# Optimization experiments

Hardware: AMD Instinct MI355X
Metric: run time of the kernel (lower is better)

## Reference

```python
import jax, jax.numpy as jnp
import numpy as np

DIM = 2048
HV = 32          # num value heads
HK = 16          # num key heads
DK = 128         # head_k_dim
DV = 128         # head_v_dim
KW = 4           # conv kernel width
KEY_DIM = HK * DK            # 2048
VAL_DIM = HV * DV            # 4096
CONV_DIM = 2 * KEY_DIM + VAL_DIM  # 8192
EPS = 1e-6
B, T = 2, 2048


def setup_inputs() -> dict:
    key = jax.random.key(0)
    ks = jax.random.split(key, 10)
    s = 0.02
    x = jax.random.normal(ks[0], (B, T, DIM), jnp.float32)
    W_qkv = jax.random.normal(ks[1], (DIM, CONV_DIM), jnp.float32) * s
    W_z = jax.random.normal(ks[2], (DIM, VAL_DIM), jnp.float32) * s
    W_a = jax.random.normal(ks[3], (DIM, HV), jnp.float32) * s
    W_b = jax.random.normal(ks[4], (DIM, HV), jnp.float32) * s
    W_out = jax.random.normal(ks[5], (VAL_DIM, DIM), jnp.float32) * s
    conv_w = jax.random.normal(ks[6], (CONV_DIM, KW), jnp.float32) * 0.2
    A_log = jnp.log(jax.random.uniform(ks[7], (HV,), jnp.float32, 1e-3, 16.0))
    dt_bias = jnp.ones((HV,), jnp.float32)
    norm_weight = jnp.ones((DV,), jnp.float32)
    return {"x": x, "W_qkv": W_qkv, "W_z": W_z, "W_a": W_a, "W_b": W_b,
            "W_out": W_out, "conv_w": conv_w, "dt_bias": dt_bias,
            "A_log": A_log, "norm_weight": norm_weight}


def _l2norm(t):
    return t * jax.lax.rsqrt(jnp.sum(t * t, axis=-1, keepdims=True) + EPS)


def _forward(x, W_qkv, W_z, W_a, W_b, W_out, conv_w, dt_bias, A_log, norm_weight):
    Bb, Tt, _ = x.shape
    mixed = x @ W_qkv                       # [B,T,CONV_DIM]
    z = x @ W_z                             # [B,T,VAL_DIM]
    a = x @ W_a                             # [B,T,HV]
    b = x @ W_b                             # [B,T,HV]

    # depthwise causal conv1d (left pad KW-1) + silu
    xp = jnp.pad(mixed, ((0, 0), (KW - 1, 0), (0, 0)))
    conv = sum(xp[:, i:i + Tt, :] * conv_w[:, i] for i in range(KW))
    mixed = jax.nn.silu(conv)

    q, k, v = jnp.split(mixed, [KEY_DIM, 2 * KEY_DIM], axis=-1)
    q = q.reshape(Bb, Tt, HK, DK)
    k = k.reshape(Bb, Tt, HK, DK)
    v = v.reshape(Bb, Tt, HV, DV)
    rep = HV // HK
    q = jnp.repeat(q, rep, axis=2)          # [B,T,HV,DK]
    k = jnp.repeat(k, rep, axis=2)

    # decay / beta
    beta = jax.nn.sigmoid(b)                                    # [B,T,HV]
    g = -jnp.exp(A_log) * jax.nn.softplus(a + dt_bias)          # [B,T,HV], < 0

    # qk l2norm in kernel + scale
    q = _l2norm(q) * (DK ** -0.5)
    k = _l2norm(k)

    # gated delta rule recurrence, time-major scan
    qT = q.transpose(1, 0, 2, 3)
    kT = k.transpose(1, 0, 2, 3)
    vT = v.transpose(1, 0, 2, 3)
    gT = g.transpose(1, 0, 2)
    bT = beta.transpose(1, 0, 2)
    S0 = jnp.zeros((Bb, HV, DK, DV), jnp.float32)

    def step(S, inp):
        qt, kt, vt, gt, bt = inp
        S = S * jnp.exp(gt)[..., None, None]
        pred = jnp.einsum('bhk,bhkv->bhv', kt, S)
        u = (vt - pred) * bt[..., None]
        S = S + jnp.einsum('bhk,bhv->bhkv', kt, u)
        o = jnp.einsum('bhk,bhkv->bhv', qt, S)
        return S, o

    _, oT = jax.lax.scan(step, S0, (qT, kT, vT, gT, bT))
    o = oT.transpose(1, 0, 2, 3)            # [B,T,HV,DV]

    # gated RMSNorm over head_v_dim: weight * rmsnorm(o) * silu(z)
    var = jnp.mean(o * o, axis=-1, keepdims=True)
    on = o * jax.lax.rsqrt(var + EPS) * norm_weight
    zg = z.reshape(Bb, Tt, HV, DV)
    on = on * jax.nn.silu(zg)

    return on.reshape(Bb, Tt, VAL_DIM) @ W_out


def reference(x, W_qkv, W_z, W_a, W_b, W_out, conv_w, dt_bias, A_log, norm_weight):
    return _forward(x, W_qkv, W_z, W_a, W_b, W_out, conv_w, dt_bias, A_log, norm_weight)
```

## Files before the change

### kernel.cpp

```cpp
#include <hip/hip_runtime.h>
#include <hip/hip_bf16.h>
#include <cstdint>
#include <cstddef>

#define DIM_ 2048
#define HV_ 32
#define HK_ 16
#define DK_ 128
#define DV_ 128
#define KW_ 4
#define KEY_DIM_ 2048
#define VAL_DIM_ 4096
#define CONV_DIM_ 8192
#define B_ 2
#define T_ 2048
#define BT_ 4096
#define CH_ 64
#define NC_ (T_ / CH_)

typedef short s8v __attribute__((ext_vector_type(8)));
typedef float f4v __attribute__((ext_vector_type(4)));

__device__ __forceinline__ unsigned short f2b(float f) {
    union { float f; unsigned u; } c; c.f = f;
    unsigned u = c.u;
    return (unsigned short)((u + 0x7fffu + ((u >> 16) & 1u)) >> 16);
}
__device__ __forceinline__ float b2f(unsigned short s) {
    union { unsigned u; float f; } c; c.u = ((unsigned)s) << 16;
    return c.f;
}
__device__ __forceinline__ unsigned int pk2(float a, float b) {
    return (unsigned)f2b(a) | ((unsigned)f2b(b) << 16);
}
__device__ __forceinline__ float silu(float x) { return x / (1.f + expf(-x)); }

__global__ void cast_bf16_k(const float* __restrict__ in, unsigned short* __restrict__ out, int n8) {
    int i = blockIdx.x * blockDim.x + threadIdx.x;
    if (i >= n8) return;
    int base = i * 8;
    f4v a = *(const f4v*)(in + base);
    f4v b = *(const f4v*)(in + base + 4);
    s8v o;
    o[0] = (short)f2b(a[0]); o[1] = (short)f2b(a[1]); o[2] = (short)f2b(a[2]); o[3] = (short)f2b(a[3]);
    o[4] = (short)f2b(b[0]); o[5] = (short)f2b(b[1]); o[6] = (short)f2b(b[2]); o[7] = (short)f2b(b[3]);
    *(s8v*)(out + base) = o;
}

__global__ void transpose_cast_k(const float* __restrict__ in, unsigned short* __restrict__ out,
                                 int R, int C) {
    __shared__ float tile[32][33];
    int c0 = blockIdx.x * 32, r0 = blockIdx.y * 32;
    int tx = threadIdx.x & 31, ty = threadIdx.x >> 5;
#pragma unroll
    for (int j = 0; j < 32; j += 8)
        tile[ty + j][tx] = in[(size_t)(r0 + ty + j) * C + c0 + tx];
    __syncthreads();
#pragma unroll
    for (int j = 0; j < 32; j += 8)
        out[(size_t)(c0 + ty + j) * R + r0 + tx] = f2b(tile[tx][ty + j]);
}

__global__ void pack_ab_k(const float* __restrict__ Wa, const float* __restrict__ Wb,
                          float* __restrict__ WabP) {
    int idx = blockIdx.x * 256 + threadIdx.x;
    int k = idx >> 6;
    int c = idx & 63;
    float v = (c < 32) ? Wa[(size_t)k * 32 + c] : Wb[(size_t)k * 32 + (c - 32)];
    WabP[((size_t)(k >> 2) * 64 + c) * 4 + (k & 3)] = v;
}

template <int OUT_BF16>
__global__ __launch_bounds__(256) void gemm_bt_k(const unsigned short* __restrict__ A,
                                                 const unsigned short* __restrict__ BT,
                                                 void* __restrict__ Cv,
                                                 int M, int N, int K) {
    __shared__ __attribute__((aligned(16))) unsigned short As[128 * 64];
    __shared__ __attribute__((aligned(16))) unsigned short Bs[128 * 64];
    const int tid = threadIdx.x;
    const int wid = tid >> 6, lane = tid & 63;
    const int wm = wid >> 1, wn = wid & 1;
    const int m0 = blockIdx.y * 128, n0 = blockIdx.x * 128;

    f4v acc[4][4];
#pragma unroll
    for (int i = 0; i < 4; i++)
#pragma unroll
        for (int j = 0; j < 4; j++) acc[i][j] = (f4v){0.f, 0.f, 0.f, 0.f};

    const int rowA = tid >> 3;
    const int cb   = (tid & 7) << 4;

    for (int kt = 0; kt < K; kt += 64) {
#pragma unroll
        for (int i = 0; i < 4; i++) {
            int row = i * 32 + rowA;
            int scb = cb ^ ((row & 7) << 4);
            const unsigned short* ga = A  + (size_t)(m0 + row) * K + kt + (scb >> 1);
            const unsigned short* gb = BT + (size_t)(n0 + row) * K + kt + (scb >> 1);
            char* la = (char*)As + i * 4096 + (wid << 10);
            char* lb = (char*)Bs + i * 4096 + (wid << 10);
            __builtin_amdgcn_global_load_lds(
                (const __attribute__((address_space(1))) unsigned int*)ga,
                (__attribute__((address_space(3))) unsigned int*)la, 16, 0, 0);
            __builtin_amdgcn_global_load_lds(
                (const __attribute__((address_space(1))) unsigned int*)gb,
                (__attribute__((address_space(3))) unsigned int*)lb, 16, 0, 0);
        }
        __syncthreads();
#pragma unroll
        for (int kk = 0; kk < 2; kk++) {
            s8v af[4], bfr[4];
#pragma unroll
            for (int mi = 0; mi < 4; mi++) {
                int row = wm * 64 + mi * 16 + (lane & 15);
                int byteoff = (row << 7) + ((kk * 64 + ((lane >> 4) << 4)) ^ ((row & 7) << 4));
                af[mi] = *(const s8v*)((const char*)As + byteoff);
            }
#pragma unroll
            for (int ni = 0; ni < 4; ni++) {
                int row = wn * 64 + ni * 16 + (lane & 15);
                int byteoff = (row << 7) + ((kk * 64 + ((lane >> 4) << 4)) ^ ((row & 7) << 4));
                bfr[ni] = *(const s8v*)((const char*)Bs + byteoff);
            }
#pragma unroll
            for (int mi = 0; mi < 4; mi++)
#pragma unroll
                for (int ni = 0; ni < 4; ni++)
                    acc[mi][ni] = __builtin_amdgcn_mfma_f32_16x16x32_bf16(
                        af[mi], bfr[ni], acc[mi][ni], 0, 0, 0);
        }
        __syncthreads();
    }
#pragma unroll
    for (int mi = 0; mi < 4; mi++) {
#pragma unroll
        for (int ni = 0; ni < 4; ni++) {
            int row = m0 + wm * 64 + mi * 16 + ((lane >> 4) << 2);
            int col = n0 + wn * 64 + ni * 16 + (lane & 15);
#pragma unroll
            for (int r = 0; r < 4; r++) {
                float v = acc[mi][ni][r];
                if (OUT_BF16)
                    ((unsigned short*)Cv)[(size_t)(row + r) * N + col] = f2b(v);
                else
                    ((float*)Cv)[(size_t)(row + r) * N + col] = v;
            }
        }
    }
}

__global__ __launch_bounds__(256) void ab_gbeta_k(const float* __restrict__ x,
                                                  const float* __restrict__ WabP,
                                                  const float* __restrict__ dt_bias,
                                                  const float* __restrict__ A_log,
                                                  float* __restrict__ g, float* __restrict__ beta) {
    const int c = threadIdx.x & 63;
    const int rg = __builtin_amdgcn_readfirstlane(threadIdx.x >> 6);
    const int row = blockIdx.x * 4 + rg;
    const float* xp = x + (size_t)row * 2048;
    const float* wp = WabP + c * 4;
    float acc0 = 0.f, acc1 = 0.f;
#pragma unroll 4
    for (int kb = 0; kb < 512; kb += 2) {
        f4v w0 = *(const f4v*)(wp + (size_t)kb * 256);
        f4v w1 = *(const f4v*)(wp + (size_t)(kb + 1) * 256);
        f4v x0 = *(const f4v*)(xp + kb * 4);
        f4v x1 = *(const f4v*)(xp + kb * 4 + 4);
        acc0 += x0[0] * w0[0] + x0[1] * w0[1] + x0[2] * w0[2] + x0[3] * w0[3];
        acc1 += x1[0] * w1[0] + x1[1] * w1[1] + x1[2] * w1[2] + x1[3] * w1[3];
    }
    float tot = acc0 + acc1;
    if (c < 32) {
        float av = tot + dt_bias[c];
        float sp = (av > 20.f) ? av : log1pf(expf(av));
        g[(size_t)row * 32 + c] = -expf(A_log[c]) * sp;
    } else {
        beta[(size_t)row * 32 + (c - 32)] = 1.f / (1.f + expf(-tot));
    }
}

__global__ __launch_bounds__(256) void conv_fused_k(const unsigned short* __restrict__ mixp,
                                                    const float* __restrict__ convw,
                                                    unsigned short* __restrict__ qn,
                                                    unsigned short* __restrict__ kn,
                                                    unsigned short* __restrict__ vv) {
    int btid = blockIdx.x;
    int t = btid & (T_ - 1);
    int c = (blockIdx.y << 9) + (threadIdx.x << 1);
    const unsigned short* base = mixp + (size_t)btid * CONV_DIM_ + c;
    unsigned m3 = *(const unsigned*)(base);
    unsigned m2 = (t >= 1) ? *(const unsigned*)(base - CONV_DIM_) : 0u;
    unsigned m1 = (t >= 2) ? *(const unsigned*)(base - 2 * CONV_DIM_) : 0u;
    unsigned m0 = (t >= 3) ? *(const unsigned*)(base - 3 * CONV_DIM_) : 0u;
    f4v w0 = *(const f4v*)(convw + (size_t)c * 4);
    f4v w1 = *(const f4v*)(convw + (size_t)c * 4 + 4);
    float v0 = b2f((unsigned short)(m3 & 0xffff)) * w0[3] + b2f((unsigned short)(m2 & 0xffff)) * w0[2]
             + b2f((unsigned short)(m1 & 0xffff)) * w0[1] + b2f((unsigned short)(m0 & 0xffff)) * w0[0];
    float v1 = b2f((unsigned short)(m3 >> 16)) * w1[3] + b2f((unsigned short)(m2 >> 16)) * w1[2]
             + b2f((unsigned short)(m1 >> 16)) * w1[1] + b2f((unsigned short)(m0 >> 16)) * w1[0];
    v0 = silu(v0); v1 = silu(v1);
    if (c < 2 * KEY_DIM_) {
        float ss = v0 * v0 + v1 * v1;
#pragma unroll
        for (int m = 1; m < 64; m <<= 1) ss += __shfl_xor(ss, m);
        float scale = rsqrtf(ss + 1e-6f);
        int head = (c >> 7) & 15, d = c & 127;
        if (c < KEY_DIM_) {
            scale *= 0.08838834764831845f;
            *(unsigned*)(qn + ((size_t)btid * HK_ + head) * DK_ + d) = pk2(v0 * scale, v1 * scale);
        } else {
            *(unsigned*)(kn + ((size_t)btid * HK_ + head) * DK_ + d) = pk2(v0 * scale, v1 * scale);
        }
    } else {
        *(unsigned*)(vv + (size_t)btid * VAL_DIM_ + (c - 2 * KEY_DIM_)) = pk2(v0, v1);
    }
}

__global__ __launch_bounds__(256) void chunk_pre_k(
    const unsigned short* __restrict__ qn, const unsigned short* __restrict__ kn,
    unsigned short* __restrict__ vv,
    const float* __restrict__ g, const float* __restrict__ beta,
    unsigned short* __restrict__ Wg, unsigned short* __restrict__ Aog,
    unsigned short* __restrict__ knT, float* __restrict__ expG, float* __restrict__ expGr)
{
    const int c = blockIdx.x, h = blockIdx.y, b = blockIdx.z;
    const int hk = h >> 1;
    const int tid = threadIdx.x, wid = tid >> 6, lane = tid & 63;
    const int r15 = lane & 15, g4 = lane >> 4;

    __shared__ __attribute__((aligned(16))) unsigned short Klds[64 * 128];
    __shared__ __attribute__((aligned(16))) unsigned short Xlds[128 * 64];
    __shared__ float AT[64][68];
    __shared__ float STmp[16][17];
    __shared__ float Gl[64], Bl[64], EG[64];

    const size_t t0 = (size_t)b * T_ + (size_t)c * 64;
    const size_t cbk = ((size_t)(b * 32 + h) * 32 + c);

#pragma unroll
    for (int p = 0; p < 4; p++) {
        int row = p * 16 + (tid >> 4);
        int colB = (tid & 15) << 4;
        int sw = colB ^ ((row & 7) << 4);
        s8v kv = *(const s8v*)(kn + ((t0 + row) * HK_ + hk) * DK_ + (colB >> 1));
        *(s8v*)((char*)Klds + row * 256 + sw) = kv;
        s8v qv = *(const s8v*)(qn + ((t0 + row) * HK_ + hk) * DK_ + (colB >> 1));
        *(s8v*)((char*)Xlds + row * 256 + sw) = qv;
    }
    if (tid < 64) {
        Gl[tid] = g[(t0 + tid) * HV_ + h];
        Bl[tid] = beta[(t0 + tid) * HV_ + h];
    }
    __syncthreads();
    if (tid == 0) {
        float s = 0.f;
        for (int i = 0; i < 64; i++) { s += Gl[i]; Gl[i] = s; }
    }
    __syncthreads();
    if (tid < 64) {
        float Gi = Gl[tid], Gn = Gl[63];
        float e1 = expf(Gi), e2 = expf(Gn - Gi);
        EG[tid] = e1;
        expG[cbk * 64 + tid] = e1;
        expGr[cbk * 64 + tid] = e2;
    }
    __syncthreads();

    f4v kkv[4], qkv[4];
#pragma unroll
    for (int jt = 0; jt < 4; jt++) { kkv[jt] = (f4v){0,0,0,0}; qkv[jt] = (f4v){0,0,0,0}; }
    const int arow = wid * 16 + r15;
#pragma unroll
    for (int ks = 0; ks < 4; ks++) {
        int abyte = arow * 256 + ((ks * 64 + (g4 << 4)) ^ ((arow & 7) << 4));
        s8v ak = *(const s8v*)((const char*)Klds + abyte);
        s8v aq = *(const s8v*)((const char*)Xlds + abyte);
#pragma unroll
        for (int jt = 0; jt < 4; jt++) {
            int jrow = jt * 16 + r15;
            int bbyte = jrow * 256 + ((ks * 64 + (g4 << 4)) ^ ((jrow & 7) << 4));
            s8v bk = *(const s8v*)((const char*)Klds + bbyte);
            kkv[jt] = __builtin_amdgcn_mfma_f32_16x16x32_bf16(ak, bk, kkv[jt], 0, 0, 0);
            qkv[jt] = __builtin_amdgcn_mfma_f32_16x16x32_bf16(aq, bk, qkv[jt], 0, 0, 0);
        }
    }
#pragma unroll
    for (int jt = 0; jt < 4; jt++) {
#pragma unroll
        for (int r = 0; r < 4; r++) {
            int i = wid * 16 + g4 * 4 + r;
            int j = jt * 16 + r15;
            float em = expf(fminf(Gl[i] - Gl[j], 0.f));
            AT[i][j] = (j < i) ? Bl[i] * em * kkv[jt][r] : 0.f;
            float ao = (j <= i) ? em * qkv[jt][r] : 0.f;
            Aog[cbk * 4096 + i * 64 + j] = f2b(ao);
        }
    }
    __syncthreads();

    for (int u = tid; u < 1024; u += 256) {
        int row = u >> 4, v0i = (u & 15) << 3;
        s8v vx = *(const s8v*)(vv + (t0 + row) * VAL_DIM_ + h * 128 + v0i);
        float bt = Bl[row];
#pragma unroll
        for (int e = 0; e < 8; e++) {
            int v = v0i + e;
            *(unsigned short*)((char*)Xlds + v * 128 + ((row * 2) ^ ((v & 7) << 4))) =
                f2b(b2f((unsigned short)vx[e]) * bt);
        }
    }
    if ((h & 1) == 0) {
        int dk = tid & 127, th = (tid >> 7) << 5;
        size_t basek = ((size_t)(b * 16 + hk) * 128 + dk) * (size_t)T_ + (size_t)c * 64 + th;
#pragma unroll
        for (int t8 = 0; t8 < 4; t8++) {
            s8v kv;
#pragma unroll
            for (int e = 0; e < 8; e++) {
                int tt = th + t8 * 8 + e;
                kv[e] = (short)*(const unsigned short*)((const char*)Klds + tt * 256 + ((dk * 2) ^ ((tt & 7) << 4)));
            }
            *(s8v*)(knT + basek + t8 * 8) = kv;
        }
    }
    __syncthreads();

    if (lane < 16) {
        int r0 = wid * 16, col = lane;
#pragma unroll
        for (int i = 0; i < 16; i++) {
            float s = 0.f;
            for (int j = 0; j < i; j++) s += AT[r0 + i][r0 + j] * AT[r0 + j][r0 + col];
            AT[r0 + i][r0 + col] = ((col == i) ? 1.f : 0.f) - s;
        }
    }
    __syncthreads();

    {
        int ii = tid >> 4, jj = tid & 15;
        for (int I = 1; I < 4; I++)
            for (int J = 0; J < I; J++) {
                float s = 0.f;
                for (int K = J; K < I; K++) {
#pragma unroll
                    for (int m = 0; m < 16; m++)
                        s += AT[16 * I + ii][16 * K + m] * AT[16 * K + m][16 * J + jj];
                }
                STmp[ii][jj] = s;
                __syncthreads();
                float y = 0.f;
#pragma unroll
                for (int m = 0; m < 16; m++) y += AT[16 * I + ii][16 * I + m] * STmp[m][jj];
                __syncthreads();
                AT[16 * I + ii][16 * J + jj] = -y;
                __syncthreads();
            }
    }

    f4v tb[8];
#pragma unroll
    for (int vt = 0; vt < 8; vt++) tb[vt] = (f4v){0,0,0,0};
#pragma unroll
    for (int ks = 0; ks < 2; ks++) {
        s8v ta;
#pragma unroll
        for (int e = 0; e < 8; e++) ta[e] = (short)f2b(AT[arow][ks * 32 + g4 * 8 + e]);
#pragma unroll
        for (int vt = 0; vt < 8; vt++) {
            int v = vt * 16 + r15;
            int bbyte = v * 128 + ((ks * 64 + (g4 << 4)) ^ ((v & 7) << 4));
            s8v bv = *(const s8v*)((const char*)Xlds + bbyte);
            tb[vt] = __builtin_amdgcn_mfma_f32_16x16x32_bf16(ta, bv, tb[vt], 0, 0, 0);
        }
    }
#pragma unroll
    for (int vt = 0; vt < 8; vt++)
#pragma unroll
        for (int r = 0; r < 4; r++) {
            int i = wid * 16 + g4 * 4 + r, v = vt * 16 + r15;
            vv[(t0 + i) * VAL_DIM_ + h * 128 + v] = f2b(tb[vt][r]);
        }
    __syncthreads();

    {
        int dk = tid & 127;
        int tb0 = (tid >> 7) << 5;
#pragma unroll
        for (int t8 = 0; t8 < 4; t8++) {
            int tbase = tb0 + t8 * 8;
            s8v kw;
#pragma unroll
            for (int e = 0; e < 8; e++) {
                int t = tbase + e;
                float kv = b2f(*(const unsigned short*)((const char*)Klds + t * 256 + ((dk * 2) ^ ((t & 7) << 4))));
                kw[e] = (short)f2b(kv * Bl[t] * EG[t]);
            }
            *(s8v*)((char*)Xlds + dk * 128 + ((tbase * 2) ^ ((dk & 7) << 4))) = kw;
        }
    }
    __syncthreads();

    f4v wm[8];
#pragma unroll
    for (int dt = 0; dt < 8; dt++) wm[dt] = (f4v){0,0,0,0};
#pragma unroll
    for (int ks = 0; ks < 2; ks++) {
        s8v ta;
#pragma unroll
        for (int e = 0; e < 8; e++) ta[e] = (short)f2b(AT[arow][ks * 32 + g4 * 8 + e]);
#pragma unroll
        for (int dt = 0; dt < 8; dt++) {
            int dkr = dt * 16 + r15;
            int bbyte = dkr * 128 + ((ks * 64 + (g4 << 4)) ^ ((dkr & 7) << 4));
            s8v bw = *(const s8v*)((const char*)Xlds + bbyte);
            wm[dt] = __builtin_amdgcn_mfma_f32_16x16x32_bf16(ta, bw, wm[dt], 0, 0, 0);
        }
    }
#pragma unroll
    for (int dt = 0; dt < 8; dt++)
#pragma unroll
        for (int r = 0; r < 4; r++) {
            int i = wid * 16 + g4 * 4 + r, dk = dt * 16 + r15;
            Wg[cbk * 8192 + i * 128 + dk] = f2b(wm[dt][r]);
        }
}

__global__ __launch_bounds__(256) void chunk_scan_k(
    const unsigned short* __restrict__ qn, const unsigned short* __restrict__ knT,
    const unsigned short* __restrict__ tbv,
    const unsigned short* __restrict__ Wg, const unsigned short* __restrict__ Aog,
    const float* __restrict__ expG, const float* __restrict__ expGr,
    unsigned short* __restrict__ ob)
{
    const int bx = blockIdx.x;
    const int vq = bx & 3, h = (bx >> 2) & 31, b = bx >> 7;
    const int hk = h >> 1;
    const int tid = threadIdx.x, wid = tid >> 6, lane = tid & 63;
    const int r15 = lane & 15, g4 = lane >> 4;

    __shared__ __attribute__((aligned(16))) unsigned short Slds[32 * 128];
    __shared__ __attribute__((aligned(16))) unsigned short Ulds[32 * 64];
    __shared__ __attribute__((aligned(16))) unsigned short Uplds[32 * 64];

    f4v S[2][2];
#pragma unroll
    for (int i = 0; i < 2; i++)
#pragma unroll
        for (int j = 0; j < 2; j++) S[i][j] = (f4v){0,0,0,0};

    struct ScanOps {
        s8v aw[4], aa[2], ak[4], q0[4];
        float tv[8], egr4[4], egi, gam;
    };
    ScanOps opA, opB;

    const unsigned short* kpbase = knT + ((size_t)(b * 16 + hk) * 128) * (size_t)T_;

    auto scan_load = [&](ScanOps& o, int c) {
        const size_t cbk = ((size_t)(b * 32 + h) * 32 + c);
        const size_t t0 = (size_t)b * T_ + (size_t)c * 64;
        const unsigned short* wp = Wg + cbk * 8192 + (size_t)(wid * 16 + r15) * 128;
#pragma unroll
        for (int ks = 0; ks < 4; ks++) o.aw[ks] = *(const s8v*)(wp + ks * 32 + g4 * 8);
        const unsigned short* ap = Aog + cbk * 4096 + (size_t)(wid * 16 + r15) * 64;
#pragma unroll
        for (int ks = 0; ks < 2; ks++) o.aa[ks] = *(const s8v*)(ap + ks * 32 + g4 * 8);
#pragma unroll
        for (int ks = 0; ks < 2; ks++)
#pragma unroll
            for (int dkt = 0; dkt < 2; dkt++)
                o.ak[ks * 2 + dkt] = *(const s8v*)(kpbase +
                    (size_t)((wid * 2 + dkt) * 16 + r15) * T_ + (size_t)c * 64 + ks * 32 + g4 * 8);
        const unsigned short* qp = qn + ((t0 + wid * 16 + r15) * HK_ + hk) * DK_;
#pragma unroll
        for (int ks = 0; ks < 4; ks++) o.q0[ks] = *(const s8v*)(qp + ks * 32 + g4 * 8);
#pragma unroll
        for (int vt = 0; vt < 2; vt++)
#pragma unroll
            for (int r = 0; r < 4; r++) {
                int t = wid * 16 + g4 * 4 + r;
                o.tv[vt * 4 + r] = b2f(tbv[(t0 + t) * VAL_DIM_ + h * 128 + vq * 32 + vt * 16 + r15]);
            }
#pragma unroll
        for (int r = 0; r < 4; r++) o.egr4[r] = expGr[cbk * 64 + wid * 16 + g4 * 4 + r];
        o.egi = expG[cbk * 64 + wid * 16 + r15];
        o.gam = expG[cbk * 64 + 63];
    };

    auto body = [&](ScanOps& o, int c) {
#pragma unroll
        for (int dkt = 0; dkt < 2; dkt++)
#pragma unroll
            for (int vt = 0; vt < 2; vt++) {
                int v = vt * 16 + r15;
                int dkb = ((wid * 2 + dkt) * 16 + g4 * 4) * 2;
                int sw = (v & 7) << 4;
                *(unsigned int*)((char*)Slds + v * 256 + ((dkb) ^ sw))     = pk2(S[dkt][vt][0], S[dkt][vt][1]);
                *(unsigned int*)((char*)Slds + v * 256 + ((dkb + 4) ^ sw)) = pk2(S[dkt][vt][2], S[dkt][vt][3]);
            }
        __syncthreads();

        f4v P[2]; P[0] = (f4v){0,0,0,0}; P[1] = (f4v){0,0,0,0};
        s8v sf[4][2];
#pragma unroll
        for (int ks = 0; ks < 4; ks++)
#pragma unroll
            for (int vt = 0; vt < 2; vt++) {
                int v = vt * 16 + r15;
                sf[ks][vt] = *(const s8v*)((const char*)Slds + v * 256 + ((ks * 64 + g4 * 16) ^ ((v & 7) << 4)));
                P[vt] = __builtin_amdgcn_mfma_f32_16x16x32_bf16(o.aw[ks], sf[ks][vt], P[vt], 0, 0, 0);
            }
#pragma unroll
        for (int vt = 0; vt < 2; vt++) {
            float uu[4], up[4];
#pragma unroll
            for (int r = 0; r < 4; r++) {
                uu[r] = o.tv[vt * 4 + r] - P[vt][r];
                up[r] = uu[r] * o.egr4[r];
            }
            int v = vt * 16 + r15;
            int tb2 = (wid * 16 + g4 * 4) * 2;
            int sw = (v & 7) << 4;
            *(unsigned int*)((char*)Ulds  + v * 128 + ((tb2) ^ sw))     = pk2(uu[0], uu[1]);
            *(unsigned int*)((char*)Ulds  + v * 128 + ((tb2 + 4) ^ sw)) = pk2(uu[2], uu[3]);
            *(unsigned int*)((char*)Uplds + v * 128 + ((tb2) ^ sw))     = pk2(up[0], up[1]);
            *(unsigned int*)((char*)Uplds + v * 128 + ((tb2 + 4) ^ sw)) = pk2(up[2], up[3]);
        }

        f4v O[2]; O[0] = (f4v){0,0,0,0}; O[1] = (f4v){0,0,0,0};
#pragma unroll
        for (int ks = 0; ks < 4; ks++) {
            s8v qg;
#pragma unroll
            for (int e = 0; e < 8; e++) qg[e] = (short)f2b(b2f((unsigned short)o.q0[ks][e]) * o.egi);
#pragma unroll
            for (int vt = 0; vt < 2; vt++)
                O[vt] = __builtin_amdgcn_mfma_f32_16x16x32_bf16(qg, sf[ks][vt], O[vt], 0, 0, 0);
        }
        __syncthreads();

#pragma unroll
        for (int ks = 0; ks < 2; ks++)
#pragma unroll
            for (int vt = 0; vt < 2; vt++) {
                int v = vt * 16 + r15;
                s8v bu = *(const s8v*)((const char*)Ulds + v * 128 + ((ks * 64 + g4 * 16) ^ ((v & 7) << 4)));
                O[vt] = __builtin_amdgcn_mfma_f32_16x16x32_bf16(o.aa[ks], bu, O[vt], 0, 0, 0);
            }
#pragma unroll
        for (int vt = 0; vt < 2; vt++)
#pragma unroll
            for (int r = 0; r < 4; r++) {
                int t = c * 64 + wid * 16 + g4 * 4 + r;
                ob[((size_t)b * T_ + t) * VAL_DIM_ + h * 128 + vq * 32 + vt * 16 + r15] = f2b(O[vt][r]);
            }

#pragma unroll
        for (int dkt = 0; dkt < 2; dkt++)
#pragma unroll
            for (int vt = 0; vt < 2; vt++) {
                S[dkt][vt][0] *= o.gam; S[dkt][vt][1] *= o.gam;
                S[dkt][vt][2] *= o.gam; S[dkt][vt][3] *= o.gam;
            }
#pragma unroll
        for (int ks = 0; ks < 2; ks++) {
            s8v bu[2];
#pragma unroll
            for (int vt = 0; vt < 2; vt++) {
                int v = vt * 16 + r15;
                bu[vt] = *(const s8v*)((const char*)Uplds + v * 128 + ((ks * 64 + g4 * 16) ^ ((v & 7) << 4)));
            }
#pragma unroll
            for (int dkt = 0; dkt < 2; dkt++)
#pragma unroll
                for (int vt = 0; vt < 2; vt++)
                    S[dkt][vt] = __builtin_amdgcn_mfma_f32_16x16x32_bf16(o.ak[ks * 2 + dkt], bu[vt], S[dkt][vt], 0, 0, 0);
        }
    };

    scan_load(opA, 0);
    for (int c = 0; c < NC_; c += 2) {
        scan_load(opB, (c + 1 < NC_) ? c + 1 : c);
        body(opA, c);
        if (c + 2 < NC_) scan_load(opA, c + 2);
        body(opB, c + 1);
    }
}

__global__ __launch_bounds__(256) void norm_gate_k(unsigned short* __restrict__ o,
                                                   const unsigned short* __restrict__ z,
                                                   const float* __restrict__ nw) {
    int lane = threadIdx.x & 63;
    size_t bh = (size_t)blockIdx.x * 4 + (threadIdx.x >> 6);
    unsigned ov = *(unsigned*)(o + bh * 128 + lane * 2);
    float v0 = b2f((unsigned short)(ov & 0xffff)), v1 = b2f((unsigned short)(ov >> 16));
    float ss = v0 * v0 + v1 * v1;
#pragma unroll
    for (int m = 1; m < 64; m <<= 1) ss += __shfl_xor(ss, m);
    float rr = rsqrtf(ss * (1.f / 128.f) + 1e-6f);
    unsigned zv = *(const unsigned*)(z + bh * 128 + lane * 2);
    float z0 = b2f((unsigned short)(zv & 0xffff)), z1 = b2f((unsigned short)(zv >> 16));
    float o0 = v0 * rr * nw[lane * 2]     * silu(z0);
    float o1 = v1 * rr * nw[lane * 2 + 1] * silu(z1);
    *(unsigned*)(o + bh * 128 + lane * 2) = pk2(o0, o1);
}

extern "C" void kernel_launch(void* const* d_in, const int* in_sizes, int n_in,
                              void* d_out, int out_size, void* d_ws, size_t ws_size,
                              hipStream_t stream) {
    const float* x      = (const float*)d_in[0];
    const float* W_qkv  = (const float*)d_in[1];
    const float* W_z    = (const float*)d_in[2];
    const float* W_a    = (const float*)d_in[3];
    const float* W_b    = (const float*)d_in[4];
    const float* W_out  = (const float*)d_in[5];
    const float* conv_w = (const float*)d_in[6];
    const float* dt_bias= (const float*)d_in[7];
    const float* A_log  = (const float*)d_in[8];
    const float* norm_w = (const float*)d_in[9];

    char* w = (char*)d_ws;
    const size_t MBc = (size_t)1 << 20;
    unsigned short* mixp  = (unsigned short*)(w);
    unsigned short* Wmat  = (unsigned short*)(w);
    unsigned short* knT   = (unsigned short*)(w + 32 * MBc);
    unsigned short* Aog   = (unsigned short*)(w + 48 * MBc);
    unsigned short* WqkvT = (unsigned short*)(w + 64 * MBc);
    unsigned short* obuf  = (unsigned short*)(w + 64 * MBc);
    unsigned short* kn    = (unsigned short*)(w + 80 * MBc);
    unsigned short* WzT   = (unsigned short*)(w + 96 * MBc);
    unsigned short* WoutT = (unsigned short*)(w + 96 * MBc);
    unsigned short* xb    = (unsigned short*)(w + 112 * MBc);
    unsigned short* qn    = (unsigned short*)(w + 112 * MBc);
    unsigned short* vv    = (unsigned short*)(w + 128 * MBc);
    unsigned short* zb    = (unsigned short*)(w + 160 * MBc);
    float* gbuf  = (float*)(w + 192 * MBc);
    float* bbuf  = (float*)(w + 192 * MBc + 512 * 1024);
    float* expG  = (float*)(w + 192 * MBc + 1024 * 1024);
    float* expGr = (float*)(w + 192 * MBc + 1536 * 1024);
    float* WabP  = (float*)(w + 194 * MBc);

    pack_ab_k<<<512, 256, 0, stream>>>(W_a, W_b, WabP);
    cast_bf16_k<<<(BT_ * DIM_ / 8 + 255) / 256, 256, 0, stream>>>(x, xb, BT_ * DIM_ / 8);
    ab_gbeta_k<<<BT_ / 4, 256, 0, stream>>>(x, WabP, dt_bias, A_log, gbuf, bbuf);
    transpose_cast_k<<<dim3(CONV_DIM_ / 32, DIM_ / 32), 256, 0, stream>>>(W_qkv, WqkvT, DIM_, CONV_DIM_);
    transpose_cast_k<<<dim3(VAL_DIM_ / 32, DIM_ / 32), 256, 0, stream>>>(W_z, WzT, DIM_, VAL_DIM_);
    gemm_bt_k<1><<<dim3(CONV_DIM_ / 256, BT_ / 128), 256, 0, stream>>>(xb, WqkvT, mixp, BT_, CONV_DIM_, DIM_);
    gemm_bt_k<1><<<dim3(CONV_DIM_ / 256, BT_ / 128), 256, 0, stream>>>(
        xb, WqkvT + (size_t)(CONV_DIM_ / 2) * DIM_, mixp + CONV_DIM_ / 2, BT_, CONV_DIM_, DIM_);
    gemm_bt_k<1><<<dim3(VAL_DIM_ / 128, BT_ / 128), 256, 0, stream>>>(xb, WzT, zb, BT_, VAL_DIM_, DIM_);
    transpose_cast_k<<<dim3(DIM_ / 32, VAL_DIM_ / 32), 256, 0, stream>>>(W_out, WoutT, VAL_DIM_, DIM_);
    conv_fused_k<<<dim3(BT_, CONV_DIM_ / 512), 256, 0, stream>>>(mixp, conv_w, qn, kn, vv);
    chunk_pre_k<<<dim3(NC_, HV_, B_), 256, 0, stream>>>(qn, kn, vv, gbuf, bbuf,
                                                        Wmat, Aog, knT, expG, expGr);
    chunk_scan_k<<<B_ * HV_ * 4, 256, 0, stream>>>(qn, knT, vv, Wmat, Aog, expG, expGr, obuf);
    norm_gate_k<<<BT_ * HV_ / 4, 256, 0, stream>>>(obuf, zb, norm_w);
    gemm_bt_k<0><<<dim3(DIM_ / 128, BT_ / 128), 256, 0, stream>>>(obuf, WoutT, d_out, BT_, DIM_, VAL_DIM_);
}
```

Baseline: 721.4 us.

## Share key-head Gram products across value-head pair and merge QKV GEMM launches

chunk_pre_k now handles both value heads that share a key head in one block. The K·K^T and Q·K^T MFMA products and the K/Q LDS loads are computed once and reused for both heads, and the grid is halved. The serial cumulative sum of g is replaced by a wave-level shuffle prefix scan. Separately, the two half-width QKV GEMM launches are merged into one launch over the full conv dimension. Each chunk_pre block now does more serial work, and with half as many blocks there is less parallelism.

```diff
diff --git a/kernel.cpp b/kernel.cpp
--- a/kernel.cpp
+++ b/kernel.cpp
@@ -224,8 +224,7 @@
     unsigned short* __restrict__ Wg, unsigned short* __restrict__ Aog,
     unsigned short* __restrict__ knT, float* __restrict__ expG, float* __restrict__ expGr)
 {
-    const int c = blockIdx.x, h = blockIdx.y, b = blockIdx.z;
-    const int hk = h >> 1;
+    const int c = blockIdx.x, hp = blockIdx.y, b = blockIdx.z;
     const int tid = threadIdx.x, wid = tid >> 6, lane = tid & 63;
     const int r15 = lane & 15, g4 = lane >> 4;
 
@@ -233,37 +232,37 @@
     __shared__ __attribute__((aligned(16))) unsigned short Xlds[128 * 64];
     __shared__ float AT[64][68];
     __shared__ float STmp[16][17];
-    __shared__ float Gl[64], Bl[64], EG[64];
+    __shared__ float Gl2[2][64], Bl2[2][64], EG2[2][64];
 
     const size_t t0 = (size_t)b * T_ + (size_t)c * 64;
-    const size_t cbk = ((size_t)(b * 32 + h) * 32 + c);
 
 #pragma unroll
     for (int p = 0; p < 4; p++) {
         int row = p * 16 + (tid >> 4);
         int colB = (tid & 15) << 4;
         int sw = colB ^ ((row & 7) << 4);
-        s8v kv = *(const s8v*)(kn + ((t0 + row) * HK_ + hk) * DK_ + (colB >> 1));
+        s8v kv = *(const s8v*)(kn + ((t0 + row) * HK_ + hp) * DK_ + (colB >> 1));
         *(s8v*)((char*)Klds + row * 256 + sw) = kv;
-        s8v qv = *(const s8v*)(qn + ((t0 + row) * HK_ + hk) * DK_ + (colB >> 1));
+        s8v qv = *(const s8v*)(qn + ((t0 + row) * HK_ + hp) * DK_ + (colB >> 1));
         *(s8v*)((char*)Xlds + row * 256 + sw) = qv;
     }
-    if (tid < 64) {
-        Gl[tid] = g[(t0 + tid) * HV_ + h];
-        Bl[tid] = beta[(t0 + tid) * HV_ + h];
-    }
-    __syncthreads();
-    if (tid == 0) {
-        float s = 0.f;
-        for (int i = 0; i < 64; i++) { s += Gl[i]; Gl[i] = s; }
-    }
-    __syncthreads();
-    if (tid < 64) {
-        float Gi = Gl[tid], Gn = Gl[63];
-        float e1 = expf(Gi), e2 = expf(Gn - Gi);
-        EG[tid] = e1;
-        expG[cbk * 64 + tid] = e1;
-        expGr[cbk * 64 + tid] = e2;
+    if (wid < 2) {
+        int h = hp * 2 + wid;
+        float v = g[(t0 + lane) * HV_ + h];
+        float bv = beta[(t0 + lane) * HV_ + h];
+#pragma unroll
+        for (int off = 1; off < 64; off <<= 1) {
+            float n = __shfl_up(v, off);
+            if (lane >= off) v += n;
+        }
+        float Gn = __shfl(v, 63);
+        float e1 = expf(v), e2 = expf(Gn - v);
+        Gl2[wid][lane] = v;
+        Bl2[wid][lane] = bv;
+        EG2[wid][lane] = e1;
+        size_t cbk = ((size_t)(b * 32 + h) * 32 + c);
+        expG[cbk * 64 + lane] = e1;
+        expGr[cbk * 64 + lane] = e2;
     }
     __syncthreads();
 
@@ -285,145 +284,152 @@
             qkv[jt] = __builtin_amdgcn_mfma_f32_16x16x32_bf16(aq, bk, qkv[jt], 0, 0, 0);
         }
     }
-#pragma unroll
-    for (int jt = 0; jt < 4; jt++) {
-#pragma unroll
-        for (int r = 0; r < 4; r++) {
-            int i = wid * 16 + g4 * 4 + r;
-            int j = jt * 16 + r15;
-            float em = expf(fminf(Gl[i] - Gl[j], 0.f));
-            AT[i][j] = (j < i) ? Bl[i] * em * kkv[jt][r] : 0.f;
-            float ao = (j <= i) ? em * qkv[jt][r] : 0.f;
-            Aog[cbk * 4096 + i * 64 + j] = f2b(ao);
-        }
-    }
-    __syncthreads();
-
-    for (int u = tid; u < 1024; u += 256) {
-        int row = u >> 4, v0i = (u & 15) << 3;
-        s8v vx = *(const s8v*)(vv + (t0 + row) * VAL_DIM_ + h * 128 + v0i);
-        float bt = Bl[row];
-#pragma unroll
-        for (int e = 0; e < 8; e++) {
-            int v = v0i + e;
-            *(unsigned short*)((char*)Xlds + v * 128 + ((row * 2) ^ ((v & 7) << 4))) =
-                f2b(b2f((unsigned short)vx[e]) * bt);
-        }
-    }
-    if ((h & 1) == 0) {
-        int dk = tid & 127, th = (tid >> 7) << 5;
-        size_t basek = ((size_t)(b * 16 + hk) * 128 + dk) * (size_t)T_ + (size_t)c * 64 + th;
-#pragma unroll
-        for (int t8 = 0; t8 < 4; t8++) {
-            s8v kv;
+
+    for (int hh = 0; hh < 2; hh++) {
+        const int h = hp * 2 + hh;
+        const size_t cbk = ((size_t)(b * 32 + h) * 32 + c);
+
+#pragma unroll
+        for (int jt = 0; jt < 4; jt++) {
+#pragma unroll
+            for (int r = 0; r < 4; r++) {
+                int i = wid * 16 + g4 * 4 + r;
+                int j = jt * 16 + r15;
+                float em = expf(fminf(Gl2[hh][i] - Gl2[hh][j], 0.f));
+                AT[i][j] = (j < i) ? Bl2[hh][i] * em * kkv[jt][r] : 0.f;
+                float ao = (j <= i) ? em * qkv[jt][r] : 0.f;
+                Aog[cbk * 4096 + i * 64 + j] = f2b(ao);
+            }
+        }
+        __syncthreads();
+
+        for (int u = tid; u < 1024; u += 256) {
+            int row = u >> 4, v0i = (u & 15) << 3;
+            s8v vx = *(const s8v*)(vv + (t0 + row) * VAL_DIM_ + h * 128 + v0i);
+            float bt = Bl2[hh][row];
 #pragma unroll
             for (int e = 0; e < 8; e++) {
-                int tt = th + t8 * 8 + e;
-                kv[e] = (short)*(const unsigned short*)((const char*)Klds + tt * 256 + ((dk * 2) ^ ((tt & 7) << 4)));
-            }
-            *(s8v*)(knT + basek + t8 * 8) = kv;
-        }
-    }
-    __syncthreads();
-
-    if (lane < 16) {
-        int r0 = wid * 16, col = lane;
-#pragma unroll
-        for (int i = 0; i < 16; i++) {
-            float s = 0.f;
-            for (int j = 0; j < i; j++) s += AT[r0 + i][r0 + j] * AT[r0 + j][r0 + col];
-            AT[r0 + i][r0 + col] = ((col == i) ? 1.f : 0.f) - s;
-        }
-    }
-    __syncthreads();
-
-    {
-        int ii = tid >> 4, jj = tid & 15;
-        for (int I = 1; I < 4; I++)
-            for (int J = 0; J < I; J++) {
+                int v = v0i + e;
+                *(unsigned short*)((char*)Xlds + v * 128 + ((row * 2) ^ ((v & 7) << 4))) =
+                    f2b(b2f((unsigned short)vx[e]) * bt);
+            }
+        }
+        if (hh == 0) {
+            int dk = tid & 127, th = (tid >> 7) << 5;
+            size_t basek = ((size_t)(b * 16 + hp) * 128 + dk) * (size_t)T_ + (size_t)c * 64 + th;
+#pragma unroll
+            for (int t8 = 0; t8 < 4; t8++) {
+                s8v kv;
+#pragma unroll
+                for (int e = 0; e < 8; e++) {
+                    int tt = th + t8 * 8 + e;
+                    kv[e] = (short)*(const unsigned short*)((const char*)Klds + tt * 256 + ((dk * 2) ^ ((tt & 7) << 4)));
+                }
+                *(s8v*)(knT + basek + t8 * 8) = kv;
+            }
+        }
+        __syncthreads();
+
+        if (lane < 16) {
+            int r0 = wid * 16, col = lane;
+#pragma unroll
+            for (int i = 0; i < 16; i++) {
                 float s = 0.f;
-                for (int K = J; K < I; K++) {
-#pragma unroll
-                    for (int m = 0; m < 16; m++)
-                        s += AT[16 * I + ii][16 * K + m] * AT[16 * K + m][16 * J + jj];
+                for (int j = 0; j < i; j++) s += AT[r0 + i][r0 + j] * AT[r0 + j][r0 + col];
+                AT[r0 + i][r0 + col] = ((col == i) ? 1.f : 0.f) - s;
+            }
+        }
+        __syncthreads();
+
+        {
+            int ii = tid >> 4, jj = tid & 15;
+            for (int I = 1; I < 4; I++)
+                for (int J = 0; J < I; J++) {
+                    float s = 0.f;
+                    for (int K = J; K < I; K++) {
+#pragma unroll
+                        for (int m = 0; m < 16; m++)
+                            s += AT[16 * I + ii][16 * K + m] * AT[16 * K + m][16 * J + jj];
+                    }
+                    STmp[ii][jj] = s;
+                    __syncthreads();
+                    float y = 0.f;
+#pragma unroll
+                    for (int m = 0; m < 16; m++) y += AT[16 * I + ii][16 * I + m] * STmp[m][jj];
+                    __syncthreads();
+                    AT[16 * I + ii][16 * J + jj] = -y;
+                    __syncthreads();
                 }
-                STmp[ii][jj] = s;
-                __syncthreads();
-                float y = 0.f;
-#pragma unroll
-                for (int m = 0; m < 16; m++) y += AT[16 * I + ii][16 * I + m] * STmp[m][jj];
-                __syncthreads();
-                AT[16 * I + ii][16 * J + jj] = -y;
-                __syncthreads();
-            }
-    }
-
-    f4v tb[8];
-#pragma unroll
-    for (int vt = 0; vt < 8; vt++) tb[vt] = (f4v){0,0,0,0};
-#pragma unroll
-    for (int ks = 0; ks < 2; ks++) {
-        s8v ta;
-#pragma unroll
-        for (int e = 0; e < 8; e++) ta[e] = (short)f2b(AT[arow][ks * 32 + g4 * 8 + e]);
-#pragma unroll
-        for (int vt = 0; vt < 8; vt++) {
-            int v = vt * 16 + r15;
-            int bbyte = v * 128 + ((ks * 64 + (g4 << 4)) ^ ((v & 7) << 4));
-            s8v bv = *(const s8v*)((const char*)Xlds + bbyte);
-            tb[vt] = __builtin_amdgcn_mfma_f32_16x16x32_bf16(ta, bv, tb[vt], 0, 0, 0);
-        }
-    }
-#pragma unroll
-    for (int vt = 0; vt < 8; vt++)
-#pragma unroll
-        for (int r = 0; r < 4; r++) {
-            int i = wid * 16 + g4 * 4 + r, v = vt * 16 + r15;
-            vv[(t0 + i) * VAL_DIM_ + h * 128 + v] = f2b(tb[vt][r]);
-        }
-    __syncthreads();
-
-    {
-        int dk = tid & 127;
-        int tb0 = (tid >> 7) << 5;
-#pragma unroll
-        for (int t8 = 0; t8 < 4; t8++) {
-            int tbase = tb0 + t8 * 8;
-            s8v kw;
-#pragma unroll
-            for (int e = 0; e < 8; e++) {
-                int t = tbase + e;
-                float kv = b2f(*(const unsigned short*)((const char*)Klds + t * 256 + ((dk * 2) ^ ((t & 7) << 4))));
-                kw[e] = (short)f2b(kv * Bl[t] * EG[t]);
-            }
-            *(s8v*)((char*)Xlds + dk * 128 + ((tbase * 2) ^ ((dk & 7) << 4))) = kw;
-        }
-    }
-    __syncthreads();
-
-    f4v wm[8];
-#pragma unroll
-    for (int dt = 0; dt < 8; dt++) wm[dt] = (f4v){0,0,0,0};
-#pragma unroll
-    for (int ks = 0; ks < 2; ks++) {
-        s8v ta;
-#pragma unroll
-        for (int e = 0; e < 8; e++) ta[e] = (short)f2b(AT[arow][ks * 32 + g4 * 8 + e]);
-#pragma unroll
-        for (int dt = 0; dt < 8; dt++) {
-            int dkr = dt * 16 + r15;
-            int bbyte = dkr * 128 + ((ks * 64 + (g4 << 4)) ^ ((dkr & 7) << 4));
-            s8v bw = *(const s8v*)((const char*)Xlds + bbyte);
-            wm[dt] = __builtin_amdgcn_mfma_f32_16x16x32_bf16(ta, bw, wm[dt], 0, 0, 0);
-        }
-    }
-#pragma unroll
-    for (int dt = 0; dt < 8; dt++)
-#pragma unroll
-        for (int r = 0; r < 4; r++) {
-            int i = wid * 16 + g4 * 4 + r, dk = dt * 16 + r15;
-            Wg[cbk * 8192 + i * 128 + dk] = f2b(wm[dt][r]);
-        }
+        }
+
+        f4v tb[8];
+#pragma unroll
+        for (int vt = 0; vt < 8; vt++) tb[vt] = (f4v){0,0,0,0};
+#pragma unroll
+        for (int ks = 0; ks < 2; ks++) {
+            s8v ta;
+#pragma unroll
+            for (int e = 0; e < 8; e++) ta[e] = (short)f2b(AT[arow][ks * 32 + g4 * 8 + e]);
+#pragma unroll
+            for (int vt = 0; vt < 8; vt++) {
+                int v = vt * 16 + r15;
+                int bbyte = v * 128 + ((ks * 64 + (g4 << 4)) ^ ((v & 7) << 4));
+                s8v bv = *(const s8v*)((const char*)Xlds + bbyte);
+                tb[vt] = __builtin_amdgcn_mfma_f32_16x16x32_bf16(ta, bv, tb[vt], 0, 0, 0);
+            }
+        }
+#pragma unroll
+        for (int vt = 0; vt < 8; vt++)
+#pragma unroll
+            for (int r = 0; r < 4; r++) {
+                int i = wid * 16 + g4 * 4 + r, v = vt * 16 + r15;
+                vv[(t0 + i) * VAL_DIM_ + h * 128 + v] = f2b(tb[vt][r]);
+            }
+        __syncthreads();
+
+        {
+            int dk = tid & 127;
+            int tb0 = (tid >> 7) << 5;
+#pragma unroll
+            for (int t8 = 0; t8 < 4; t8++) {
+                int tbase = tb0 + t8 * 8;
+                s8v kw;
+#pragma unroll
+                for (int e = 0; e < 8; e++) {
+                    int t = tbase + e;
+                    float kv = b2f(*(const unsigned short*)((const char*)Klds + t * 256 + ((dk * 2) ^ ((t & 7) << 4))));
+                    kw[e] = (short)f2b(kv * Bl2[hh][t] * EG2[hh][t]);
+                }
+                *(s8v*)((char*)Xlds + dk * 128 + ((tbase * 2) ^ ((dk & 7) << 4))) = kw;
+            }
+        }
+        __syncthreads();
+
+        f4v wm[8];
+#pragma unroll
+        for (int dt = 0; dt < 8; dt++) wm[dt] = (f4v){0,0,0,0};
+#pragma unroll
+        for (int ks = 0; ks < 2; ks++) {
+            s8v ta;
+#pragma unroll
+            for (int e = 0; e < 8; e++) ta[e] = (short)f2b(AT[arow][ks * 32 + g4 * 8 + e]);
+#pragma unroll
+            for (int dt = 0; dt < 8; dt++) {
+                int dkr = dt * 16 + r15;
+                int bbyte = dkr * 128 + ((ks * 64 + (g4 << 4)) ^ ((dkr & 7) << 4));
+                s8v bw = *(const s8v*)((const char*)Xlds + bbyte);
+                wm[dt] = __builtin_amdgcn_mfma_f32_16x16x32_bf16(ta, bw, wm[dt], 0, 0, 0);
+            }
+        }
+#pragma unroll
+        for (int dt = 0; dt < 8; dt++)
+#pragma unroll
+            for (int r = 0; r < 4; r++) {
+                int i = wid * 16 + g4 * 4 + r, dk = dt * 16 + r15;
+                Wg[cbk * 8192 + i * 128 + dk] = f2b(wm[dt][r]);
+            }
+        __syncthreads();
+    }
 }
 
 __global__ __launch_bounds__(256) void chunk_scan_k(
@@ -646,14 +652,12 @@
     ab_gbeta_k<<<BT_ / 4, 256, 0, stream>>>(x, WabP, dt_bias, A_log, gbuf, bbuf);
     transpose_cast_k<<<dim3(CONV_DIM_ / 32, DIM_ / 32), 256, 0, stream>>>(W_qkv, WqkvT, DIM_, CONV_DIM_);
     transpose_cast_k<<<dim3(VAL_DIM_ / 32, DIM_ / 32), 256, 0, stream>>>(W_z, WzT, DIM_, VAL_DIM_);
-    gemm_bt_k<1><<<dim3(CONV_DIM_ / 256, BT_ / 128), 256, 0, stream>>>(xb, WqkvT, mixp, BT_, CONV_DIM_, DIM_);
-    gemm_bt_k<1><<<dim3(CONV_DIM_ / 256, BT_ / 128), 256, 0, stream>>>(
-        xb, WqkvT + (size_t)(CONV_DIM_ / 2) * DIM_, mixp + CONV_DIM_ / 2, BT_, CONV_DIM_, DIM_);
+    gemm_bt_k<1><<<dim3(CONV_DIM_ / 128, BT_ / 128), 256, 0, stream>>>(xb, WqkvT, mixp, BT_, CONV_DIM_, DIM_);
     gemm_bt_k<1><<<dim3(VAL_DIM_ / 128, BT_ / 128), 256, 0, stream>>>(xb, WzT, zb, BT_, VAL_DIM_, DIM_);
     transpose_cast_k<<<dim3(DIM_ / 32, VAL_DIM_ / 32), 256, 0, stream>>>(W_out, WoutT, VAL_DIM_, DIM_);
     conv_fused_k<<<dim3(BT_, CONV_DIM_ / 512), 256, 0, stream>>>(mixp, conv_w, qn, kn, vv);
-    chunk_pre_k<<<dim3(NC_, HV_, B_), 256, 0, stream>>>(qn, kn, vv, gbuf, bbuf,
-                                                        Wmat, Aog, knT, expG, expGr);
+    chunk_pre_k<<<dim3(NC_, HV_ / 2, B_), 256, 0, stream>>>(qn, kn, vv, gbuf, bbuf,
+                                                            Wmat, Aog, knT, expG, expGr);
     chunk_scan_k<<<B_ * HV_ * 4, 256, 0, stream>>>(qn, knT, vv, Wmat, Aog, expG, expGr, obuf);
     norm_gate_k<<<BT_ * HV_ / 4, 256, 0, stream>>>(obuf, zb, norm_w);
     gemm_bt_k<0><<<dim3(DIM_ / 128, BT_ / 128), 256, 0, stream>>>(obuf, WoutT, d_out, BT_, DIM_, VAL_DIM_);
```

After: 699.5 us. -3.0%, faster.
